# Kernel optimization log

Hardware: AMD Instinct MI355X
Metric: run time of the kernel (lower is better)

The kernel has to match this reference:

```python
import jax, jax.numpy as jnp
import numpy as np

EPS = 1e-08
ITERATIONS = 3


def squash(s):
    # s: [..., d]
    s2 = jnp.sum(s * s, axis=-1, keepdims=True)
    return s2 / (1.0 + s2) * (s / jnp.sqrt(s2 + EPS))


def setup_inputs() -> dict:
    key = jax.random.key(0)
    k1, k2 = jax.random.split(key)
    B, IN_CAPS, OUT_CAPS, IN_D, OUT_D = 256, 1152, 10, 8, 16
    u = jax.random.normal(k1, (B, IN_CAPS, IN_D), dtype=jnp.float32)
    weight = jax.random.normal(k2, (IN_CAPS, OUT_CAPS, IN_D, OUT_D), dtype=jnp.float32)
    return {"u": u, "weight": weight}


def reference(u, weight):
    # u: [B, in_caps, in_d]; weight: [in_caps, out_caps, in_d, out_d]
    u_hat = jnp.einsum('ijnm,bin->bijm', weight, u)  # [B, in_caps, out_caps, out_d]
    B, in_caps, out_caps, _ = u_hat.shape
    b = jnp.zeros((B, in_caps, out_caps), dtype=u.dtype)
    v = None
    for _ in range(ITERATIONS):
        c = jax.nn.softmax(b, axis=1)  # softmax over in_caps (dim=1, faithful to source)
        s = jnp.einsum('bij,bijm->bjm', c, u_hat)  # [B, out_caps, out_d]
        v = squash(s)
        a = jnp.einsum('bjm,bijm->bij', v, u_hat)
        b = b + a
    return v
```

## Files before the change

### kernel.cpp

```cpp
#include <hip/hip_runtime.h>
#include <hip/hip_bf16.h>
#include <math.h>


#define IC 1152
#define OC 10
#define NB 256
#define TILE_DW (IC * 8)

#define NW_DW (IC * OC * 64)
#define NU_DW (NB * IC * 4)
#define WS_NEED ((size_t)(NW_DW + NU_DW) * 4)

typedef float v2f __attribute__((ext_vector_type(2)));
typedef _Float16 h2 __attribute__((ext_vector_type(2)));

#if defined(__has_builtin)
#if __has_builtin(__builtin_amdgcn_fdot2)
#define HAVE_FDOT2 1
#endif
#endif

__device__ __forceinline__ float fdot2f(unsigned w, unsigned uu, float c) {
    h2 a = *(h2*)&w, b = *(h2*)&uu;
#ifdef HAVE_FDOT2
    return __builtin_amdgcn_fdot2(a, b, c, false);
#else
    return c + (float)a.x * (float)b.x + (float)a.y * (float)b.y;
#endif
}
__device__ __forceinline__ v2f h_v2(unsigned w) {
    h2 h = *(h2*)&w;
    v2f r = {(float)h.x, (float)h.y};
    return r;
}
__device__ __forceinline__ unsigned packh2(float a, float b) {
    h2 h = {(_Float16)a, (_Float16)b};
    return *(unsigned*)&h;
}
__device__ __forceinline__ unsigned short pack1(float a) {
    __hip_bfloat16 h = __float2bfloat16(a);
    return *(unsigned short*)&h;
}

__global__ void convert_kernel(const float* __restrict__ u,
                               const float* __restrict__ W,
                               unsigned* __restrict__ ws, int do_u) {
    const int tid = blockIdx.x * blockDim.x + threadIdx.x;
    if (tid < NW_DW) {
        const int k = tid & 3, mp = (tid >> 2) & 3, q = (tid >> 4) & 3, ij = tid >> 6;
        const int m = (q << 2) + mp;
        const float* s = W + ((size_t)ij << 7) + m + (k << 5);
        ws[tid] = packh2(s[0], s[16]);
    } else if (do_u) {
        const int e = tid - NW_DW;
        if (e < NU_DW) {
            const int pr = e & 3, bi = e >> 2;
            const float* s = u + ((size_t)bi << 3) + (pr << 1);
            ws[NW_DW + e] = packh2(s[0], s[1]);
        }
    }
}

template<bool UF16>
__global__ __launch_bounds__(1024, 8)
void caps_route_kernel(const float* __restrict__ u,
                       const unsigned* __restrict__ Wh,
                       const unsigned* __restrict__ ug,
                       float* __restrict__ out) {
    extern __shared__ unsigned smem_u[];
    unsigned* uh = smem_u;
    unsigned short* ce = (unsigned short*)(uh + 2 * TILE_DW);
    float* spart = (float*)(ce + 2 * IC);

    const int t    = threadIdx.x;
    const int bx   = blockIdx.x;
    const int lane = t & 63;
    const int wid  = t >> 6;

    int x = bx & 7, sg = bx >> 3;
    int j, p;
    if (sg < 128) { j = x; p = sg; }
    else { int s2 = sg - 128; j = 8 + (x >> 2); p = ((x & 3) << 5) + s2; }
    const int bb = p * 2;

    {
        const int q  = t & 3;
        const int i0 = t >> 2;
        const int pb = (((q >> 1) ^ ((i0 >> 2) & 1)) << 2) + ((q & 1) << 1);
        const float* u0p = u + (size_t)bb * (IC * 8);
        const uint4* ua4 = (const uint4*)ug + (size_t)bb * IC;
        const uint4* ub4 = ua4 + IC;

        auto stage = [&](int i) {
            const uint4* wq4 = (const uint4*)Wh + (((size_t)(i * OC + j) << 2) + q) * 4;
            uint4 Ua, Ub;
            if constexpr (UF16) {
                Ua = ua4[i];
                Ub = ub4[i];
            } else {
                const float4 a0 = *(const float4*)(u0p + i * 8);
                const float4 a1 = *(const float4*)(u0p + i * 8 + 4);
                const float4 b0 = *(const float4*)(u0p + IC * 8 + i * 8);
                const float4 b1 = *(const float4*)(u0p + IC * 8 + i * 8 + 4);
                Ua = make_uint4(packh2(a0.x, a0.y), packh2(a0.z, a0.w),
                                packh2(a1.x, a1.y), packh2(a1.z, a1.w));
                Ub = make_uint4(packh2(b0.x, b0.y), packh2(b0.z, b0.w),
                                packh2(b1.x, b1.y), packh2(b1.z, b1.w));
            }
            const uint4 w0 = wq4[0], w1 = wq4[1], w2 = wq4[2], w3 = wq4[3];
            float A0, A1, A2, A3, B0, B1, B2, B3;
#define DOT8(acc, wm) \
            acc = fdot2f(wm.x, Ua.x, 0.f);  acc = fdot2f(wm.y, Ua.y, acc); \
            acc = fdot2f(wm.z, Ua.z, acc);  acc = fdot2f(wm.w, Ua.w, acc);
#define DOT8B(acc, wm) \
            acc = fdot2f(wm.x, Ub.x, 0.f);  acc = fdot2f(wm.y, Ub.y, acc); \
            acc = fdot2f(wm.z, Ub.z, acc);  acc = fdot2f(wm.w, Ub.w, acc);
            DOT8(A0, w0) DOT8(A1, w1) DOT8(A2, w2) DOT8(A3, w3)
            DOT8B(B0, w0) DOT8B(B1, w1) DOT8B(B2, w2) DOT8B(B3, w3)
#undef DOT8
#undef DOT8B
            const int dst = (i << 3) + pb;
            *(uint2*)&uh[dst]           = make_uint2(packh2(A0, A1), packh2(A2, A3));
            *(uint2*)&uh[TILE_DW + dst] = make_uint2(packh2(B0, B1), packh2(B2, B3));
        };
#pragma unroll
        for (int k = 0; k < 4; ++k) stage(i0 + 256 * k);
        if (i0 < IC - 1024) stage(i0 + 1024);
    }

    __syncthreads();

    const int bt = wid >> 3;
    const int w8 = wid & 7;
    const int rowbase = w8 * 144;
    const unsigned* uhT = uh + bt * TILE_DW;
    unsigned short* ceT = ce + bt * IC;

    const int mqc = lane & 3;
    const int h   = lane >> 2;
    const int pbS = (((mqc >> 1) ^ ((h >> 2) & 1)) << 2) + ((mqc & 1) << 1);
    const bool eB = ((lane >> 2) & 1) != 0;
    const int sA0 = eB ? 2 : 0, sA1 = eB ? 3 : 1;
    const int sB0 = eB ? 0 : 2, sB1 = eB ? 1 : 3;

    float L[3];
#pragma unroll
    for (int k = 0; k < 3; ++k) L[k] = 0.f;
    float se = 0.f;
    float4 vq;

    for (int r = 0; r < 3; ++r) {
        v2f aA = {0.f, 0.f}, aB = {0.f, 0.f};
        if (r == 0) {
#pragma unroll 3
            for (int k = 0; k < 9; ++k) {
                const int i = rowbase + 16 * k + h;
                const uint2 d = *(const uint2*)&uhT[(i << 3) + pbS];
                aA += h_v2(d.x);
                aB += h_v2(d.y);
            }
        } else {
#pragma unroll 3
            for (int k = 0; k < 9; ++k) {
                const int i = rowbase + 16 * k + h;
                const uint2 d = *(const uint2*)&uhT[(i << 3) + pbS];
                const float c = __uint_as_float(((unsigned)ceT[i]) << 16);
                const v2f cs = {c, c};
                aA += cs * h_v2(d.x);
                aB += cs * h_v2(d.y);
            }
        }
        float4 acc = make_float4(aA.x, aA.y, aB.x, aB.y);
#pragma unroll
        for (int o = 4; o <= 32; o <<= 1) {
            acc.x += __shfl_xor(acc.x, o, 64); acc.y += __shfl_xor(acc.y, o, 64);
            acc.z += __shfl_xor(acc.z, o, 64); acc.w += __shfl_xor(acc.w, o, 64);
        }
        float* spR = spart + (r & 1) * 320 + bt * 160;
        if (lane < 4) *(float4*)&spR[w8 * 20 + (lane << 2)] = acc;
        else if (r > 0 && lane == 4) spR[w8 * 20 + 16] = se;
        __syncthreads();

        {
            float4 ss = {0.f, 0.f, 0.f, 0.f};
            float sesum = 0.f;
#pragma unroll
            for (int s8 = 0; s8 < 8; ++s8) {
                const float4 qq = *(const float4*)&spR[s8 * 20 + (mqc << 2)];
                ss.x += qq.x; ss.y += qq.y; ss.z += qq.z; ss.w += qq.w;
                sesum += spR[s8 * 20 + 16];
            }
            const float inv = (r == 0) ? (1.0f / (float)IC) : 1.0f / sesum;
            const float4 s4 = make_float4(ss.x * inv, ss.y * inv, ss.z * inv, ss.w * inv);
            float p2 = s4.x*s4.x + s4.y*s4.y + s4.z*s4.z + s4.w*s4.w;
            p2 += __shfl_xor(p2, 1, 64);
            p2 += __shfl_xor(p2, 2, 64);
            const float sc = p2 / ((1.0f + p2) * sqrtf(p2 + 1e-8f));
            vq = make_float4(s4.x * sc, s4.y * sc, s4.z * sc, s4.w * sc);
        }

        if (r == 2) {
            if (w8 == 0 && lane < 4)
                *(float4*)&out[((size_t)(bb + bt) * OC + j) * 16 + (lane << 2)] = vq;
        } else {
            const unsigned p01 = packh2(vq.x, vq.y), p23 = packh2(vq.z, vq.w);
            const unsigned vh0 = __shfl((int)p01, sA0, 4), vh1 = __shfl((int)p23, sA0, 4);
            const unsigned vh2 = __shfl((int)p01, sA1, 4), vh3 = __shfl((int)p23, sA1, 4);
            const unsigned vh4 = __shfl((int)p01, sB0, 4), vh5 = __shfl((int)p23, sB0, 4);
            const unsigned vh6 = __shfl((int)p01, sB1, 4), vh7 = __shfl((int)p23, sB1, 4);
            se = 0.f;
#define BROW(i, Lk) {                                                     \
            const uint4 da = *(const uint4*)&uhT[(i) << 3];               \
            const uint4 db = *(const uint4*)&uhT[((i) << 3) + 4];         \
            float dpA = fdot2f(da.x, vh0, 0.f);                           \
            dpA = fdot2f(da.y, vh1, dpA);                                 \
            dpA = fdot2f(da.z, vh2, dpA);                                 \
            dpA = fdot2f(da.w, vh3, dpA);                                 \
            float dpB = fdot2f(db.x, vh4, 0.f);                           \
            dpB = fdot2f(db.y, vh5, dpB);                                 \
            dpB = fdot2f(db.z, vh6, dpB);                                 \
            dpB = fdot2f(db.w, vh7, dpB);                                 \
            Lk += dpA + dpB;                                              \
            const float ev = __expf(Lk);   \
            ceT[i] = pack1(ev);                                           \
            se += ev; }
            BROW(rowbase + lane, L[0])
            BROW(rowbase + lane + 64, L[1])
            if (lane < 16) { BROW(rowbase + 128 + lane, L[2]) }
#undef BROW
#pragma unroll
            for (int o = 32; o >= 1; o >>= 1) se += __shfl_xor(se, o, 64);
        }
    }
}

extern "C" void kernel_launch(void* const* d_in, const int* in_sizes, int n_in,
                              void* d_out, int out_size, void* d_ws, size_t ws_size,
                              hipStream_t stream) {
    const float* u = (const float*)d_in[0];
    const float* W = (const float*)d_in[1];
    float* out = (float*)d_out;
    unsigned* ws = (unsigned*)d_ws;

    const int do_u = (ws_size >= WS_NEED) ? 1 : 0;
    const int total = NW_DW + (do_u ? NU_DW : 0);
    convert_kernel<<<(total + 255) / 256, 256, 0, stream>>>(u, W, ws, do_u);

    const size_t shmem = (size_t)2 * TILE_DW * 4
                       + (size_t)2 * IC * 2
                       + 640 * 4;
    if (do_u) {
        hipFuncSetAttribute((const void*)caps_route_kernel<true>,
                            hipFuncAttributeMaxDynamicSharedMemorySize, (int)shmem);
        caps_route_kernel<true><<<(NB / 2) * OC, 1024, shmem, stream>>>(u, ws, ws + NW_DW, out);
    } else {
        hipFuncSetAttribute((const void*)caps_route_kernel<false>,
                            hipFuncAttributeMaxDynamicSharedMemorySize, (int)shmem);
        caps_route_kernel<false><<<(NB / 2) * OC, 1024, shmem, stream>>>(u, ws, ws + NW_DW, out);
    }
}
```

Measured before the change: 112.4 us.

## Keep u_hat rows in registers and reduce with fp16 butterfly shuffles

The routing kernel drops its large LDS tile for u_hat. Each thread now holds its three input-capsule rows in registers, blocks shrink to 512 threads, and the weight layout is reordered so loads across lanes are coalesced. Per-wave partial sums are reduced with packed fp16 shuffle trees and combined through a small LDS buffer using per-wave max-rescaled softmax, so there is one barrier per iteration. The aim is to remove LDS traffic and shared-memory occupancy limits, at the cost of heavier register use and more fp16 accumulation error.

```diff
diff --git a/kernel.cpp b/kernel.cpp
--- a/kernel.cpp
+++ b/kernel.cpp
@@ -6,9 +6,8 @@
 #define IC 1152
 #define OC 10
 #define NB 256
-#define TILE_DW (IC * 8)
-
-#define NW_DW (IC * OC * 64)
+
+#define NW_DW (18 * OC * 16 * 256)
 #define NU_DW (NB * IC * 4)
 #define WS_NEED ((size_t)(NW_DW + NU_DW) * 4)
 
@@ -38,9 +37,12 @@
     h2 h = {(_Float16)a, (_Float16)b};
     return *(unsigned*)&h;
 }
-__device__ __forceinline__ unsigned short pack1(float a) {
-    __hip_bfloat16 h = __float2bfloat16(a);
-    return *(unsigned short*)&h;
+__device__ __forceinline__ unsigned h2u(h2 v) { return *(unsigned*)&v; }
+__device__ __forceinline__ h2 u2h(unsigned v) { return *(h2*)&v; }
+__device__ __forceinline__ h2 hshfl_xor(h2 v, int m) {
+    unsigned b = *(unsigned*)&v;
+    unsigned r = (unsigned)__shfl_xor((int)b, m, 64);
+    return *(h2*)&r;
 }
 
 __global__ void convert_kernel(const float* __restrict__ u,
@@ -48,9 +50,10 @@
                                unsigned* __restrict__ ws, int do_u) {
     const int tid = blockIdx.x * blockDim.x + threadIdx.x;
     if (tid < NW_DW) {
-        const int k = tid & 3, mp = (tid >> 2) & 3, q = (tid >> 4) & 3, ij = tid >> 6;
-        const int m = (q << 2) + mp;
-        const float* s = W + ((size_t)ij << 7) + m + (k << 5);
+        const int kn = tid & 3, lg = (tid >> 2) & 63, k = (tid >> 8) & 15;
+        const int rest = tid >> 12, j = rest % OC, g = rest / OC;
+        const int i = (g << 6) + lg;
+        const float* s = W + (((size_t)(i * OC + j)) << 7) + (kn << 5) + k;
         ws[tid] = packh2(s[0], s[16]);
     } else if (do_u) {
         const int e = tid - NW_DW;
@@ -63,15 +66,13 @@
 }
 
 template<bool UF16>
-__global__ __launch_bounds__(1024, 8)
+__global__ __launch_bounds__(512, 2)
 void caps_route_kernel(const float* __restrict__ u,
                        const unsigned* __restrict__ Wh,
                        const unsigned* __restrict__ ug,
                        float* __restrict__ out) {
-    extern __shared__ unsigned smem_u[];
-    unsigned* uh = smem_u;
-    unsigned short* ce = (unsigned short*)(uh + 2 * TILE_DW);
-    float* spart = (float*)(ce + 2 * IC);
+    __shared__ unsigned spart[2 * 144];
+    __shared__ unsigned vbuf[8 * 16];
 
     const int t    = threadIdx.x;
     const int bx   = blockIdx.x;
@@ -81,157 +82,210 @@
     int x = bx & 7, sg = bx >> 3;
     int j, p;
     if (sg < 128) { j = x; p = sg; }
-    else { int s2 = sg - 128; j = 8 + (x >> 2); p = ((x & 3) << 5) + s2; }
+    else { int s2v = sg - 128; j = 8 + (x >> 2); p = ((x & 3) << 5) + s2v; }
     const int bb = p * 2;
 
+    const int g3  = 16 + (wid >> 2);
+    const int lg3 = ((wid & 3) << 4) + lane;
+    const int i1  = (wid << 6) + lane;
+    const int i2  = 512 + i1;
+    const int i3  = (g3 << 6) + lg3;
+
+    unsigned uhA[3][8], uhB[3][8];
+
+    auto rowcalc = [&](int g, int lgv, uint4 Ua, uint4 Ub, unsigned* rA, unsigned* rB) {
+        const uint4* wp = (const uint4*)Wh + (size_t)(g * OC + j) * 1024 + lgv;
+#pragma unroll
+        for (int pp = 0; pp < 8; ++pp) {
+            const uint4 w0 = wp[(2 * pp) * 64];
+            const uint4 w1 = wp[(2 * pp + 1) * 64];
+            float A0 = fdot2f(w0.x, Ua.x, 0.f); A0 = fdot2f(w0.y, Ua.y, A0);
+            A0 = fdot2f(w0.z, Ua.z, A0);        A0 = fdot2f(w0.w, Ua.w, A0);
+            float A1 = fdot2f(w1.x, Ua.x, 0.f); A1 = fdot2f(w1.y, Ua.y, A1);
+            A1 = fdot2f(w1.z, Ua.z, A1);        A1 = fdot2f(w1.w, Ua.w, A1);
+            float B0 = fdot2f(w0.x, Ub.x, 0.f); B0 = fdot2f(w0.y, Ub.y, B0);
+            B0 = fdot2f(w0.z, Ub.z, B0);        B0 = fdot2f(w0.w, Ub.w, B0);
+            float B1 = fdot2f(w1.x, Ub.x, 0.f); B1 = fdot2f(w1.y, Ub.y, B1);
+            B1 = fdot2f(w1.z, Ub.z, B1);        B1 = fdot2f(w1.w, Ub.w, B1);
+            rA[pp] = packh2(A0, A1);
+            rB[pp] = packh2(B0, B1);
+        }
+    };
+
+    auto fetchU = [&](int i, uint4& Ua, uint4& Ub) {
+        if constexpr (UF16) {
+            const uint4* ua4 = (const uint4*)ug + (size_t)bb * IC;
+            Ua = ua4[i];
+            Ub = ua4[IC + i];
+        } else {
+            const float* u0p = u + (size_t)bb * (IC * 8);
+            const float4 a0 = *(const float4*)(u0p + i * 8);
+            const float4 a1 = *(const float4*)(u0p + i * 8 + 4);
+            const float4 b0 = *(const float4*)(u0p + IC * 8 + i * 8);
+            const float4 b1 = *(const float4*)(u0p + IC * 8 + i * 8 + 4);
+            Ua = make_uint4(packh2(a0.x, a0.y), packh2(a0.z, a0.w),
+                            packh2(a1.x, a1.y), packh2(a1.z, a1.w));
+            Ub = make_uint4(packh2(b0.x, b0.y), packh2(b0.z, b0.w),
+                            packh2(b1.x, b1.y), packh2(b1.z, b1.w));
+        }
+    };
+
+    auto tree8 = [&](h2* s) -> h2 {
+        const bool b5 = (lane & 32) != 0, b4 = (lane & 16) != 0, b3 = (lane & 8) != 0;
+        h2 tq[4];
+#pragma unroll
+        for (int q = 0; q < 4; ++q) {
+            h2 snd = b5 ? s[q] : s[q + 4];
+            tq[q] = (b5 ? s[q + 4] : s[q]) + hshfl_xor(snd, 32);
+        }
+        h2 uq[2];
+#pragma unroll
+        for (int q = 0; q < 2; ++q) {
+            h2 snd = b4 ? tq[q] : tq[q + 2];
+            uq[q] = (b4 ? tq[q + 2] : tq[q]) + hshfl_xor(snd, 16);
+        }
+        h2 xq;
+        {
+            h2 snd = b3 ? uq[0] : uq[1];
+            xq = (b3 ? uq[1] : uq[0]) + hshfl_xor(snd, 8);
+        }
+        xq += hshfl_xor(xq, 4);
+        xq += hshfl_xor(xq, 2);
+        xq += hshfl_xor(xq, 1);
+        return xq;
+    };
+
+    const int sel = lane & 7;
+
     {
-        const int q  = t & 3;
-        const int i0 = t >> 2;
-        const int pb = (((q >> 1) ^ ((i0 >> 2) & 1)) << 2) + ((q & 1) << 1);
-        const float* u0p = u + (size_t)bb * (IC * 8);
-        const uint4* ua4 = (const uint4*)ug + (size_t)bb * IC;
-        const uint4* ub4 = ua4 + IC;
-
-        auto stage = [&](int i) {
-            const uint4* wq4 = (const uint4*)Wh + (((size_t)(i * OC + j) << 2) + q) * 4;
-            uint4 Ua, Ub;
-            if constexpr (UF16) {
-                Ua = ua4[i];
-                Ub = ub4[i];
-            } else {
-                const float4 a0 = *(const float4*)(u0p + i * 8);
-                const float4 a1 = *(const float4*)(u0p + i * 8 + 4);
-                const float4 b0 = *(const float4*)(u0p + IC * 8 + i * 8);
-                const float4 b1 = *(const float4*)(u0p + IC * 8 + i * 8 + 4);
-                Ua = make_uint4(packh2(a0.x, a0.y), packh2(a0.z, a0.w),
-                                packh2(a1.x, a1.y), packh2(a1.z, a1.w));
-                Ub = make_uint4(packh2(b0.x, b0.y), packh2(b0.z, b0.w),
-                                packh2(b1.x, b1.y), packh2(b1.z, b1.w));
+        uint4 Ua, Ub;
+        fetchU(i1, Ua, Ub);
+        rowcalc(wid, lane, Ua, Ub, uhA[0], uhB[0]);
+        fetchU(i2, Ua, Ub);
+        rowcalc(8 + wid, lane, Ua, Ub, uhA[1], uhB[1]);
+        if (lane < 16) {
+            fetchU(i3, Ua, Ub);
+            rowcalc(g3, lg3, Ua, Ub, uhA[2], uhB[2]);
+        } else {
+#pragma unroll
+            for (int pp = 0; pp < 8; ++pp) { uhA[2][pp] = 0u; uhB[2][pp] = 0u; }
+        }
+        h2 sa[8], sb[8];
+#pragma unroll
+        for (int pp = 0; pp < 8; ++pp) {
+            sa[pp] = u2h(uhA[0][pp]) + u2h(uhA[1][pp]) + u2h(uhA[2][pp]);
+            sb[pp] = u2h(uhB[0][pp]) + u2h(uhB[1][pp]) + u2h(uhB[2][pp]);
+        }
+        h2 ta = tree8(sa), tb = tree8(sb);
+        if (sel < 2)
+            spart[16 + sel * 64 + (lane >> 3) * 8 + wid] = sel ? h2u(tb) : h2u(ta);
+        else if (sel == 2) spart[wid] = packh2(0.f, 0.f);
+        else if (sel == 3) spart[8 + wid] = packh2(144.f, 144.f);
+    }
+
+    __syncthreads();
+
+    float LA[3], LB[3];
+    LA[0] = 0.f; LA[1] = 0.f; LA[2] = (lane < 16) ? 0.f : -1e30f;
+    LB[0] = 0.f; LB[1] = 0.f; LB[2] = (lane < 16) ? 0.f : -1e30f;
+
+    const int cp = lane & 7, cbt = (lane >> 3) & 1;
+
+    for (int r = 0; r < 3; ++r) {
+        const int pi = (r & 1) * 144;
+        const uint4 q0 = *(const uint4*)&spart[pi + 16 + cbt * 64 + cp * 8];
+        const uint4 q1 = *(const uint4*)&spart[pi + 16 + cbt * 64 + cp * 8 + 4];
+        const uint4 m0 = *(const uint4*)&spart[pi];
+        const uint4 m1 = *(const uint4*)&spart[pi + 4];
+        const uint4 e0 = *(const uint4*)&spart[pi + 8];
+        const uint4 e1 = *(const uint4*)&spart[pi + 12];
+        v2f s2 = {0.f, 0.f};
+        float ses = 0.f;
+#define CW(qc, mc, ec) {                                                  \
+        const h2 mh = u2h(mc); const h2 eh = u2h(ec);                     \
+        const float fac = __expf((float)(cbt ? mh.y : mh.x));             \
+        const v2f pv = h_v2(qc);                                          \
+        s2.x += pv.x * fac; s2.y += pv.y * fac;                           \
+        ses += (float)(cbt ? eh.y : eh.x) * fac; }
+        CW(q0.x, m0.x, e0.x) CW(q0.y, m0.y, e0.y)
+        CW(q0.z, m0.z, e0.z) CW(q0.w, m0.w, e0.w)
+        CW(q1.x, m1.x, e1.x) CW(q1.y, m1.y, e1.y)
+        CW(q1.z, m1.z, e1.z) CW(q1.w, m1.w, e1.w)
+#undef CW
+        const float inv = 1.0f / ses;
+        const float sx = s2.x * inv, sy = s2.y * inv;
+        float p2 = sx * sx + sy * sy;
+        p2 += __shfl_xor(p2, 1, 64);
+        p2 += __shfl_xor(p2, 2, 64);
+        p2 += __shfl_xor(p2, 4, 64);
+        const float sc = p2 / ((1.0f + p2) * sqrtf(p2 + 1e-8f));
+        const float vx = sx * sc, vy = sy * sc;
+
+        if (r == 2) {
+            if (lane < 16)
+                *(float2*)&out[((size_t)(bb + cbt) * OC + j) * 16 + (cp << 1)] =
+                    make_float2(vx, vy);
+            break;
+        }
+
+        if (lane < 16) vbuf[(wid << 4) + lane] = packh2(vx, vy);
+        asm volatile("s_waitcnt lgkmcnt(0)" ::: "memory");
+
+        const uint4 va0 = *(const uint4*)&vbuf[(wid << 4)];
+        const uint4 va1 = *(const uint4*)&vbuf[(wid << 4) + 4];
+        const uint4 vb0 = *(const uint4*)&vbuf[(wid << 4) + 8];
+        const uint4 vb1 = *(const uint4*)&vbuf[(wid << 4) + 12];
+#define DP8(Lk, U, A0, A1) { float d = fdot2f((U)[0], (A0).x, 0.f);       \
+        d = fdot2f((U)[1], (A0).y, d); d = fdot2f((U)[2], (A0).z, d);     \
+        d = fdot2f((U)[3], (A0).w, d); d = fdot2f((U)[4], (A1).x, d);     \
+        d = fdot2f((U)[5], (A1).y, d); d = fdot2f((U)[6], (A1).z, d);     \
+        d = fdot2f((U)[7], (A1).w, d); (Lk) += d; }
+        DP8(LA[0], uhA[0], va0, va1)
+        DP8(LA[1], uhA[1], va0, va1)
+        DP8(LA[2], uhA[2], va0, va1)
+        DP8(LB[0], uhB[0], vb0, vb1)
+        DP8(LB[1], uhB[1], vb0, vb1)
+        DP8(LB[2], uhB[2], vb0, vb1)
+#undef DP8
+        float MA = fmaxf(LA[0], fmaxf(LA[1], LA[2]));
+        float MB = fmaxf(LB[0], fmaxf(LB[1], LB[2]));
+#pragma unroll
+        for (int o = 32; o >= 1; o >>= 1) {
+            MA = fmaxf(MA, __shfl_xor(MA, o, 64));
+            MB = fmaxf(MB, __shfl_xor(MB, o, 64));
+        }
+        const unsigned mdw = packh2(MA, MB);
+        const h2 mh2 = u2h(mdw);
+        const float MAu = (float)mh2.x, MBu = (float)mh2.y;
+
+        h2 sa[8], sb[8];
+#pragma unroll
+        for (int pp = 0; pp < 8; ++pp) { sa[pp] = (h2){0.f, 0.f}; sb[pp] = (h2){0.f, 0.f}; }
+        float seA = 0.f, seB = 0.f;
+#pragma unroll
+        for (int r3 = 0; r3 < 3; ++r3) {
+            const float evA = __expf(LA[r3] - MAu);
+            const float evB = __expf(LB[r3] - MBu);
+            seA += evA; seB += evB;
+            const h2 ca = u2h(packh2(evA, evA));
+            const h2 cb = u2h(packh2(evB, evB));
+#pragma unroll
+            for (int pp = 0; pp < 8; ++pp) {
+                sa[pp] += u2h(uhA[r3][pp]) * ca;
+                sb[pp] += u2h(uhB[r3][pp]) * cb;
             }
-            const uint4 w0 = wq4[0], w1 = wq4[1], w2 = wq4[2], w3 = wq4[3];
-            float A0, A1, A2, A3, B0, B1, B2, B3;
-#define DOT8(acc, wm) \
-            acc = fdot2f(wm.x, Ua.x, 0.f);  acc = fdot2f(wm.y, Ua.y, acc); \
-            acc = fdot2f(wm.z, Ua.z, acc);  acc = fdot2f(wm.w, Ua.w, acc);
-#define DOT8B(acc, wm) \
-            acc = fdot2f(wm.x, Ub.x, 0.f);  acc = fdot2f(wm.y, Ub.y, acc); \
-            acc = fdot2f(wm.z, Ub.z, acc);  acc = fdot2f(wm.w, Ub.w, acc);
-            DOT8(A0, w0) DOT8(A1, w1) DOT8(A2, w2) DOT8(A3, w3)
-            DOT8B(B0, w0) DOT8B(B1, w1) DOT8B(B2, w2) DOT8B(B3, w3)
-#undef DOT8
-#undef DOT8B
-            const int dst = (i << 3) + pb;
-            *(uint2*)&uh[dst]           = make_uint2(packh2(A0, A1), packh2(A2, A3));
-            *(uint2*)&uh[TILE_DW + dst] = make_uint2(packh2(B0, B1), packh2(B2, B3));
-        };
-#pragma unroll
-        for (int k = 0; k < 4; ++k) stage(i0 + 256 * k);
-        if (i0 < IC - 1024) stage(i0 + 1024);
-    }
-
-    __syncthreads();
-
-    const int bt = wid >> 3;
-    const int w8 = wid & 7;
-    const int rowbase = w8 * 144;
-    const unsigned* uhT = uh + bt * TILE_DW;
-    unsigned short* ceT = ce + bt * IC;
-
-    const int mqc = lane & 3;
-    const int h   = lane >> 2;
-    const int pbS = (((mqc >> 1) ^ ((h >> 2) & 1)) << 2) + ((mqc & 1) << 1);
-    const bool eB = ((lane >> 2) & 1) != 0;
-    const int sA0 = eB ? 2 : 0, sA1 = eB ? 3 : 1;
-    const int sB0 = eB ? 0 : 2, sB1 = eB ? 1 : 3;
-
-    float L[3];
-#pragma unroll
-    for (int k = 0; k < 3; ++k) L[k] = 0.f;
-    float se = 0.f;
-    float4 vq;
-
-    for (int r = 0; r < 3; ++r) {
-        v2f aA = {0.f, 0.f}, aB = {0.f, 0.f};
-        if (r == 0) {
-#pragma unroll 3
-            for (int k = 0; k < 9; ++k) {
-                const int i = rowbase + 16 * k + h;
-                const uint2 d = *(const uint2*)&uhT[(i << 3) + pbS];
-                aA += h_v2(d.x);
-                aB += h_v2(d.y);
-            }
-        } else {
-#pragma unroll 3
-            for (int k = 0; k < 9; ++k) {
-                const int i = rowbase + 16 * k + h;
-                const uint2 d = *(const uint2*)&uhT[(i << 3) + pbS];
-                const float c = __uint_as_float(((unsigned)ceT[i]) << 16);
-                const v2f cs = {c, c};
-                aA += cs * h_v2(d.x);
-                aB += cs * h_v2(d.y);
-            }
-        }
-        float4 acc = make_float4(aA.x, aA.y, aB.x, aB.y);
-#pragma unroll
-        for (int o = 4; o <= 32; o <<= 1) {
-            acc.x += __shfl_xor(acc.x, o, 64); acc.y += __shfl_xor(acc.y, o, 64);
-            acc.z += __shfl_xor(acc.z, o, 64); acc.w += __shfl_xor(acc.w, o, 64);
-        }
-        float* spR = spart + (r & 1) * 320 + bt * 160;
-        if (lane < 4) *(float4*)&spR[w8 * 20 + (lane << 2)] = acc;
-        else if (r > 0 && lane == 4) spR[w8 * 20 + 16] = se;
+        }
+        h2 seh = u2h(packh2(seA, seB));
+#pragma unroll
+        for (int o = 32; o >= 1; o >>= 1) seh += hshfl_xor(seh, o);
+
+        const h2 ta = tree8(sa), tb = tree8(sb);
+        const int po = ((r + 1) & 1) * 144;
+        if (sel < 2)
+            spart[po + 16 + sel * 64 + (lane >> 3) * 8 + wid] = sel ? h2u(tb) : h2u(ta);
+        else if (sel == 2) spart[po + wid] = mdw;
+        else if (sel == 3) spart[po + 8 + wid] = h2u(seh);
         __syncthreads();
-
-        {
-            float4 ss = {0.f, 0.f, 0.f, 0.f};
-            float sesum = 0.f;
-#pragma unroll
-            for (int s8 = 0; s8 < 8; ++s8) {
-                const float4 qq = *(const float4*)&spR[s8 * 20 + (mqc << 2)];
-                ss.x += qq.x; ss.y += qq.y; ss.z += qq.z; ss.w += qq.w;
-                sesum += spR[s8 * 20 + 16];
-            }
-            const float inv = (r == 0) ? (1.0f / (float)IC) : 1.0f / sesum;
-            const float4 s4 = make_float4(ss.x * inv, ss.y * inv, ss.z * inv, ss.w * inv);
-            float p2 = s4.x*s4.x + s4.y*s4.y + s4.z*s4.z + s4.w*s4.w;
-            p2 += __shfl_xor(p2, 1, 64);
-            p2 += __shfl_xor(p2, 2, 64);
-            const float sc = p2 / ((1.0f + p2) * sqrtf(p2 + 1e-8f));
-            vq = make_float4(s4.x * sc, s4.y * sc, s4.z * sc, s4.w * sc);
-        }
-
-        if (r == 2) {
-            if (w8 == 0 && lane < 4)
-                *(float4*)&out[((size_t)(bb + bt) * OC + j) * 16 + (lane << 2)] = vq;
-        } else {
-            const unsigned p01 = packh2(vq.x, vq.y), p23 = packh2(vq.z, vq.w);
-            const unsigned vh0 = __shfl((int)p01, sA0, 4), vh1 = __shfl((int)p23, sA0, 4);
-            const unsigned vh2 = __shfl((int)p01, sA1, 4), vh3 = __shfl((int)p23, sA1, 4);
-            const unsigned vh4 = __shfl((int)p01, sB0, 4), vh5 = __shfl((int)p23, sB0, 4);
-            const unsigned vh6 = __shfl((int)p01, sB1, 4), vh7 = __shfl((int)p23, sB1, 4);
-            se = 0.f;
-#define BROW(i, Lk) {                                                     \
-            const uint4 da = *(const uint4*)&uhT[(i) << 3];               \
-            const uint4 db = *(const uint4*)&uhT[((i) << 3) + 4];         \
-            float dpA = fdot2f(da.x, vh0, 0.f);                           \
-            dpA = fdot2f(da.y, vh1, dpA);                                 \
-            dpA = fdot2f(da.z, vh2, dpA);                                 \
-            dpA = fdot2f(da.w, vh3, dpA);                                 \
-            float dpB = fdot2f(db.x, vh4, 0.f);                           \
-            dpB = fdot2f(db.y, vh5, dpB);                                 \
-            dpB = fdot2f(db.z, vh6, dpB);                                 \
-            dpB = fdot2f(db.w, vh7, dpB);                                 \
-            Lk += dpA + dpB;                                              \
-            const float ev = __expf(Lk);   \
-            ceT[i] = pack1(ev);                                           \
-            se += ev; }
-            BROW(rowbase + lane, L[0])
-            BROW(rowbase + lane + 64, L[1])
-            if (lane < 16) { BROW(rowbase + 128 + lane, L[2]) }
-#undef BROW
-#pragma unroll
-            for (int o = 32; o >= 1; o >>= 1) se += __shfl_xor(se, o, 64);
-        }
     }
 }
 
@@ -247,16 +301,8 @@
     const int total = NW_DW + (do_u ? NU_DW : 0);
     convert_kernel<<<(total + 255) / 256, 256, 0, stream>>>(u, W, ws, do_u);
 
-    const size_t shmem = (size_t)2 * TILE_DW * 4
-                       + (size_t)2 * IC * 2
-                       + 640 * 4;
-    if (do_u) {
-        hipFuncSetAttribute((const void*)caps_route_kernel<true>,
-                            hipFuncAttributeMaxDynamicSharedMemorySize, (int)shmem);
-        caps_route_kernel<true><<<(NB / 2) * OC, 1024, shmem, stream>>>(u, ws, ws + NW_DW, out);
-    } else {
-        hipFuncSetAttribute((const void*)caps_route_kernel<false>,
-                            hipFuncAttributeMaxDynamicSharedMemorySize, (int)shmem);
-        caps_route_kernel<false><<<(NB / 2) * OC, 1024, shmem, stream>>>(u, ws, ws + NW_DW, out);
-    }
-}
+    if (do_u)
+        caps_route_kernel<true><<<(NB / 2) * OC, 512, 0, stream>>>(u, ws, ws + NW_DW, out);
+    else
+        caps_route_kernel<false><<<(NB / 2) * OC, 512, 0, stream>>>(u, ws, ws + NW_DW, out);
+}
```

Result: slower. 124.5 us (+10.8%).
